# Kernel tuning notes

Hardware: AMD Instinct MI355X
Metric: run time of the kernel (lower is better)

Reference implementation:

```python
import jax, jax.numpy as jnp
import numpy as np

EPS = 1e-5

def mvn(feat):
    # instance norm with unbiased variance (torch .var default, correction=1)
    b, c, h, w = feat.shape
    x = feat.reshape(b, c, h * w)
    mean = x.mean(axis=2, keepdims=True)
    var = x.var(axis=2, ddof=1, keepdims=True) + EPS
    return ((x - mean) / jnp.sqrt(var)).reshape(b, c, h, w)

def conv1x1(x, w, bias):
    # x: [b,c,h,w], w: [o,c], bias: [o]
    return jnp.einsum('bchw,oc->bohw', x, w) + bias[None, :, None, None]

def setup_inputs() -> dict:
    key = jax.random.key(0)
    ks = jax.random.split(key, 10)
    C = 512
    content = jax.random.normal(ks[0], (4, C, 64, 64), dtype=jnp.float32)
    style = jax.random.normal(ks[1], (4, C, 64, 64), dtype=jnp.float32)
    s = 1.0 / np.sqrt(C)
    return {
        'content': content, 'style': style,
        'f_w': jax.random.normal(ks[2], (C, C), dtype=jnp.float32) * s,
        'f_b': jnp.zeros((C,), dtype=jnp.float32),
        'g_w': jax.random.normal(ks[3], (C, C), dtype=jnp.float32) * s,
        'g_b': jnp.zeros((C,), dtype=jnp.float32),
        'h_w': jax.random.normal(ks[4], (C, C), dtype=jnp.float32) * s,
        'h_b': jnp.zeros((C,), dtype=jnp.float32),
        'o_w': jax.random.normal(ks[5], (C, C), dtype=jnp.float32) * s,
        'o_b': jnp.zeros((C,), dtype=jnp.float32),
    }

def reference(content, style, f_w, f_b, g_w, g_b, h_w, h_b, o_w, o_b):
    b, c, hh, ww = content.shape
    F = conv1x1(mvn(content), f_w, f_b).reshape(b, c, hh * ww)   # [b,c,Nc]
    G = conv1x1(mvn(style), g_w, g_b).reshape(b, c, -1)          # [b,c,Ns]
    H = conv1x1(style, h_w, h_b).reshape(b, c, -1)               # [b,c,Ns]
    S = jnp.einsum('bcq,bcs->bqs', F, G)                          # [b,Nc,Ns]
    S = jax.nn.softmax(S, axis=-1)
    O = jnp.einsum('bcs,bqs->bcq', H, S).reshape(b, c, hh, ww)
    return conv1x1(O, o_w, o_b) + content
```

## Files before the change

### kernel.cpp

```cpp
#include <hip/hip_runtime.h>

constexpr int Cc = 512;
constexpr int Nn = 4096;
constexpr int Bb = 4;
#define EPS 1e-5f

using f16x8 = __attribute__((ext_vector_type(8))) _Float16;
using f32x4 = __attribute__((ext_vector_type(4))) float;
typedef unsigned short us;
typedef unsigned long long ull;

__device__ __forceinline__ us f2h(float f) {
    union { _Float16 h; us u; } v; v.h = (_Float16)f;
    return v.u;
}
__device__ __forceinline__ void gload_lds16(const void* g, void* l) {
    __builtin_amdgcn_global_load_lds(
        (const __attribute__((address_space(1))) void*)g,
        (__attribute__((address_space(3))) void*)l, 16, 0, 0);
}

__global__ __launch_bounds__(256) void stats2_kernel(const float* __restrict__ x0,
                                                     const float* __restrict__ x1,
                                                     float* __restrict__ mean0,
                                                     float* __restrict__ rstd0,
                                                     float* __restrict__ mean1,
                                                     float* __restrict__ rstd1) {
    int bc = blockIdx.x;
    const float* row;
    float *mean, *rstd;
    int idx;
    if (bc < Bb * Cc) { idx = bc; row = x0 + (size_t)idx * Nn; mean = mean0; rstd = rstd0; }
    else              { idx = bc - Bb * Cc; row = x1 + (size_t)idx * Nn; mean = mean1; rstd = rstd1; }
    float s = 0.f, sq = 0.f;
    for (int i = threadIdx.x * 4; i < Nn; i += 256 * 4) {
        float4 v = *reinterpret_cast<const float4*>(row + i);
        s  += v.x + v.y + v.z + v.w;
        sq += v.x*v.x + v.y*v.y + v.z*v.z + v.w*v.w;
    }
    for (int off = 32; off; off >>= 1) {
        s  += __shfl_down(s, off);
        sq += __shfl_down(sq, off);
    }
    __shared__ float ls[4], lsq[4];
    int wid = threadIdx.x >> 6;
    if ((threadIdx.x & 63) == 0) { ls[wid] = s; lsq[wid] = sq; }
    __syncthreads();
    if (threadIdx.x == 0) {
        float S  = ls[0] + ls[1] + ls[2] + ls[3];
        float SQ = lsq[0] + lsq[1] + lsq[2] + lsq[3];
        float m  = S / (float)Nn;
        float var = (SQ - S * m) / (float)(Nn - 1);
        mean[idx] = m;
        rstd[idx] = rsqrtf(var + EPS);
    }
}

__global__ __launch_bounds__(256) void pack_T(const float* __restrict__ X,
                                              const float* __restrict__ mean,
                                              const float* __restrict__ rstd,
                                              us* __restrict__ T0) {
    int b = blockIdx.z;
    int n0 = blockIdx.x * 64, c0 = blockIdx.y * 64;
    __shared__ float tile[64][65];
    const float* Xb = X + (size_t)b * Cc * Nn;
    for (int i = threadIdx.x; i < 64 * 64; i += 256) {
        int c = i >> 6, n = i & 63;
        float v = Xb[(size_t)(c0 + c) * Nn + n0 + n];
        int cg = b * Cc + c0 + c;
        tile[c][n] = (v - mean[cg]) * rstd[cg];
    }
    __syncthreads();
    us* Pb = T0 + (size_t)b * Nn * Cc;
    for (int i = threadIdx.x; i < 64 * 64; i += 256) {
        int n = i >> 6, c = i & 63;
        Pb[(size_t)(n0 + n) * Cc + c0 + c] = f2h(tile[c][n]);
    }
}

__global__ __launch_bounds__(256) void pack_style(const float* __restrict__ X,
                                                  const float* __restrict__ mean,
                                                  const float* __restrict__ rstd,
                                                  us* __restrict__ SNo,
                                                  us* __restrict__ SRo) {
    int b = blockIdx.z;
    int n0 = blockIdx.x * 64, c0 = blockIdx.y * 64;
    __shared__ float tile[64][65];
    const float* Xb = X + (size_t)b * Cc * Nn;
    for (int i = threadIdx.x; i < 64 * 64; i += 256) {
        int c = i >> 6, n = i & 63;
        tile[c][n] = Xb[(size_t)(c0 + c) * Nn + n0 + n];
    }
    __syncthreads();
    us* Nb = SNo + (size_t)b * Nn * Cc;
    us* Rb = SRo + (size_t)b * Nn * Cc;
    for (int i = threadIdx.x; i < 64 * 64; i += 256) {
        int n = i >> 6, c = i & 63;
        float raw = tile[c][n];
        int cg = b * Cc + c0 + c;
        size_t off = (size_t)(n0 + n) * Cc + c0 + c;
        Rb[off] = f2h(raw);
        Nb[off] = f2h((raw - mean[cg]) * rstd[cg]);
    }
}

__global__ __launch_bounds__(256) void pack_w(const float* __restrict__ fw, const float* __restrict__ gw,
                                              const float* __restrict__ hw, const float* __restrict__ ow,
                                              us* __restrict__ fo, us* __restrict__ go,
                                              us* __restrict__ ho, us* __restrict__ oo) {
    int i = blockIdx.x * 256 + threadIdx.x;
    if (i >= Cc * Cc) return;
    fo[i] = f2h(fw[i]);
    go[i] = f2h(gw[i]);
    ho[i] = f2h(hw[i]);
    oo[i] = f2h(ow[i]);
}

template <int EPI, int BIAS, bool RESID, int BM, int BN, int BK, int SWZ>
__global__ __launch_bounds__(256) void mfma_gemm(
    const us* __restrict__ A, int lda, long long strideA,
    const us* __restrict__ B, int ldb, long long strideB,
    void* __restrict__ out0, int ldc, long long strideC,
    const float* __restrict__ bias, const float* __restrict__ resid, long long strideR,
    int K) {
    constexpr int WM = BM / 2, WN = BN / 2;
    constexpr int MI = WM / 16, NI = WN / 16;
    constexpr int AE = BM * BK, BE = BN * BK;
    constexpr int BUFSZ = AE + BE;
    constexpr int ACH = AE / 512, BCH = BE / 512;
    __shared__ __attribute__((aligned(16))) us smem[2 * BUFSZ];

    int bz = blockIdx.z;
    const us* Ab = A + (size_t)bz * strideA;
    const us* Bbp = B + (size_t)bz * strideB;

    int bx = blockIdx.x, by = blockIdx.y;
    if constexpr (SWZ == 1) {
        int nwg = gridDim.x * gridDim.y;
        int bid = blockIdx.x + gridDim.x * blockIdx.y;
        int cpx = nwg >> 3;
        int swz = (bid & 7) * cpx + (bid >> 3);
        bx = swz % gridDim.x;
        by = swz / gridDim.x;
    } else if constexpr (SWZ == 2) {
        int bid = blockIdx.x + gridDim.x * blockIdx.y;
        int xcd = bid & 7;
        int idx = bid >> 3;
        int rpr = gridDim.y >> 2;
        int cpr = gridDim.x >> 1;
        int row0 = (xcd >> 1) * rpr;
        int col0 = (xcd & 1) * cpr;
        by = row0 + idx / cpr;
        bx = col0 + idx % cpr;
    }
    int m0 = by * BM, n0 = bx * BN;
    int tid = threadIdx.x, wave = tid >> 6, lane = tid & 63;
    int wr = wave >> 1, wc = wave & 1;
    int lr = lane & 15, lg = lane >> 4;

    auto stage = [&](int buf, int k0) {
        us* Asb = smem + buf * BUFSZ;
        us* Bsb = Asb + AE;
#pragma unroll
        for (int ch = wave; ch < ACH; ch += 4) {
            int e0 = ch * 512 + lane * 8;
            int kb = e0 / (BM * 32);
            int rem = e0 - kb * (BM * 32);
            int rr = rem >> 5;
            int gslot = ((rem & 31) >> 3) ^ ((rr >> 1) & 3);
            gload_lds16(Ab + (size_t)(m0 + rr) * lda + k0 + kb * 32 + gslot * 8,
                        Asb + ch * 512);
        }
#pragma unroll
        for (int ch = wave; ch < BCH; ch += 4) {
            int e0 = ch * 512 + lane * 8;
            int kb = e0 / (BN * 32);
            int rem = e0 - kb * (BN * 32);
            int rr = rem >> 5;
            int gslot = ((rem & 31) >> 3) ^ ((rr >> 1) & 3);
            gload_lds16(Bbp + (size_t)(n0 + rr) * ldb + k0 + kb * 32 + gslot * 8,
                        Bsb + ch * 512);
        }
    };

    f32x4 acc[MI][NI];
#pragma unroll
    for (int i = 0; i < MI; ++i)
#pragma unroll
        for (int j = 0; j < NI; ++j) acc[i][j] = (f32x4){0.f, 0.f, 0.f, 0.f};

    stage(0, 0);
    asm volatile("s_waitcnt vmcnt(0)" ::: "memory");
    __syncthreads();

    int nsteps = K / BK;
    for (int t = 0; t < nsteps; ++t) {
        int cur = t & 1;
        if (t + 1 < nsteps) stage(cur ^ 1, (t + 1) * BK);
        const us* As = smem + cur * BUFSZ;
        const us* Bs = As + AE;
#pragma unroll
        for (int kb = 0; kb < BK / 32; ++kb) {
            const us* Abase = As + kb * BM * 32;
            const us* Bbase = Bs + kb * BN * 32;
            f16x8 a[MI], b[NI];
#pragma unroll
            for (int x = 0; x < MI; ++x) {
                int row = wr * WM + x * 16 + lr;
                a[x] = *reinterpret_cast<const f16x8*>(
                    &Abase[row * 32 + ((lg ^ ((row >> 1) & 3)) << 3)]);
            }
#pragma unroll
            for (int x = 0; x < NI; ++x) {
                int row = wc * WN + x * 16 + lr;
                b[x] = *reinterpret_cast<const f16x8*>(
                    &Bbase[row * 32 + ((lg ^ ((row >> 1) & 3)) << 3)]);
            }
#pragma unroll
            for (int mi = 0; mi < MI; ++mi)
#pragma unroll
                for (int ni = 0; ni < NI; ++ni)
                    acc[mi][ni] = __builtin_amdgcn_mfma_f32_16x16x32_f16(a[mi], b[ni], acc[mi][ni], 0, 0, 0);
        }
        asm volatile("s_waitcnt vmcnt(0)" ::: "memory");
        __syncthreads();
    }

    constexpr int SP = BN + 4;
    float* sst = reinterpret_cast<float*>(smem);
    constexpr int CSEG = BN / 8;
    int rl = tid >> 3;
    int cb = (tid & 7) * CSEG;
#pragma unroll
    for (int mi = 0; mi < MI; ++mi) {
        __syncthreads();
#pragma unroll
        for (int ni = 0; ni < NI; ++ni) {
#pragma unroll
            for (int r = 0; r < 4; ++r)
                sst[(wr * 16 + lg * 4 + r) * SP + wc * WN + ni * 16 + lr] = acc[mi][ni][r];
        }
        __syncthreads();
        int grow = m0 + (rl >> 4) * WM + mi * 16 + (rl & 15);
        float bs = 0.f;
        if constexpr (BIAS == 1) bs = bias[grow];
#pragma unroll
        for (int j = 0; j < CSEG / 4; ++j) {
            int col = n0 + cb + j * 4;
            float4 v = *reinterpret_cast<const float4*>(&sst[rl * SP + cb + j * 4]);
            if constexpr (BIAS == 1) { v.x += bs; v.y += bs; v.z += bs; v.w += bs; }
            if constexpr (BIAS == 2) {
                const float4 bv = *reinterpret_cast<const float4*>(&bias[col]);
                v.x += bv.x; v.y += bv.y; v.z += bv.z; v.w += bv.w;
            }
            size_t off = (size_t)bz * strideC + (size_t)grow * ldc + col;
            if constexpr (RESID) {
                const float4 rr4 = *reinterpret_cast<const float4*>(
                    &resid[(size_t)bz * strideR + (size_t)grow * ldc + col]);
                v.x += rr4.x; v.y += rr4.y; v.z += rr4.z; v.w += rr4.w;
            }
            if constexpr (EPI == 0) {
                *reinterpret_cast<float4*>(&((float*)out0)[off]) = v;
            } else {
                ull pk = (ull)f2h(v.x) | ((ull)f2h(v.y) << 16)
                       | ((ull)f2h(v.z) << 32) | ((ull)f2h(v.w) << 48);
                *reinterpret_cast<ull*>(&((us*)out0)[off]) = pk;
            }
        }
    }
}

__global__ __launch_bounds__(256) void softmax_kernel(us* __restrict__ S) {
    us* rowp = S + (size_t)blockIdx.y * ((size_t)Nn * Nn) + (size_t)blockIdx.x * Nn;
    f16x8* r8 = reinterpret_cast<f16x8*>(rowp);
    int t = threadIdx.x;
    float f[16];
    float mx = -1e30f;
#pragma unroll
    for (int j = 0; j < 2; ++j) {
        f16x8 v = r8[t + 256 * j];
#pragma unroll
        for (int e = 0; e < 8; ++e) {
            f[j * 8 + e] = (float)v[e];
            mx = fmaxf(mx, f[j * 8 + e]);
        }
    }
    for (int off = 32; off; off >>= 1) mx = fmaxf(mx, __shfl_down(mx, off));
    __shared__ float redm[4], reds[4];
    int wid = t >> 6;
    if ((t & 63) == 0) redm[wid] = mx;
    __syncthreads();
    mx = fmaxf(fmaxf(redm[0], redm[1]), fmaxf(redm[2], redm[3]));
    float s = 0.f;
#pragma unroll
    for (int j = 0; j < 16; ++j) {
        f[j] = __expf(f[j] - mx);
        s += f[j];
    }
    for (int off = 32; off; off >>= 1) s += __shfl_down(s, off);
    if ((t & 63) == 0) reds[wid] = s;
    __syncthreads();
    s = reds[0] + reds[1] + reds[2] + reds[3];
    float inv = 1.f / s;
#pragma unroll
    for (int j = 0; j < 2; ++j) {
        f16x8 o;
#pragma unroll
        for (int e = 0; e < 8; ++e) o[e] = (_Float16)(f[j * 8 + e] * inv);
        r8[t + 256 * j] = o;
    }
}

extern "C" void kernel_launch(void* const* d_in, const int* in_sizes, int n_in,
                              void* d_out, int out_size, void* d_ws, size_t ws_size,
                              hipStream_t stream) {
    const float* content = (const float*)d_in[0];
    const float* style   = (const float*)d_in[1];
    const float* f_w = (const float*)d_in[2];
    const float* f_b = (const float*)d_in[3];
    const float* g_w = (const float*)d_in[4];
    const float* g_b = (const float*)d_in[5];
    const float* h_w = (const float*)d_in[6];
    const float* h_b = (const float*)d_in[7];
    const float* o_w = (const float*)d_in[8];
    const float* o_b = (const float*)d_in[9];
    float* out = (float*)d_out;
    char* ws = (char*)d_ws;

    const size_t PB   = (size_t)Cc * Nn;
    const size_t TEN  = PB * Bb;
    const size_t SMAT = (size_t)Nn * Nn;

    us* FT  = (us*)ws;
    us* GT  = FT + TEN;
    us* Hbf = GT + TEN;
    us* OT  = Hbf + TEN;
    us* fwh = OT + TEN;
    us* gwh = fwh + Cc * Cc;
    us* hwb = gwh + Cc * Cc;
    us* owb = hwb + Cc * Cc;
    float* meanC = (float*)(owb + Cc * Cc);
    float* rstdC = meanC + Bb * Cc;
    float* meanS = rstdC + Bb * Cc;
    float* rstdS = meanS + Bb * Cc;
    us* CN = (us*)(rstdS + Bb * Cc);
    us* SN = CN + TEN;
    us* SR = SN + TEN;
    us* S4 = CN;

    stats2_kernel<<<2 * Bb * Cc, 256, 0, stream>>>(content, style,
                                                   meanC, rstdC, meanS, rstdS);

    dim3 pgrid(Nn / 64, Cc / 64, Bb);
    pack_T<<<pgrid, 256, 0, stream>>>(content, meanC, rstdC, CN);
    pack_style<<<pgrid, 256, 0, stream>>>(style, meanS, rstdS, SN, SR);
    pack_w<<<(Cc * Cc + 255) / 256, 256, 0, stream>>>(f_w, g_w, h_w, o_w,
                                                      fwh, gwh, hwb, owb);

    mfma_gemm<1, 2, false, 64, 64, 64, 1><<<dim3(Cc / 64, Nn / 64, Bb), 256, 0, stream>>>(
        CN, Cc, (long long)PB, fwh, Cc, 0,
        FT, Cc, (long long)PB, f_b, nullptr, 0, Cc);
    mfma_gemm<1, 2, false, 64, 64, 64, 1><<<dim3(Cc / 64, Nn / 64, Bb), 256, 0, stream>>>(
        SN, Cc, (long long)PB, gwh, Cc, 0,
        GT, Cc, (long long)PB, g_b, nullptr, 0, Cc);
    mfma_gemm<1, 1, false, 64, 64, 64, 1><<<dim3(Nn / 64, Cc / 64, Bb), 256, 0, stream>>>(
        hwb, Cc, 0, SR, Cc, (long long)PB,
        Hbf, Nn, (long long)PB, h_b, nullptr, 0, Cc);

    mfma_gemm<1, 0, false, 128, 128, 32, 2><<<dim3(32, 32, Bb), 256, 0, stream>>>(
        FT, Cc, (long long)PB, GT, Cc, (long long)PB,
        S4, Nn, (long long)SMAT, nullptr, nullptr, 0, Cc);
    softmax_kernel<<<dim3(Nn, Bb), 256, 0, stream>>>(S4);
    mfma_gemm<1, 0, false, 128, 128, 64, 2><<<dim3(Cc / 128, Nn / 128, Bb), 256, 0, stream>>>(
        S4, Nn, (long long)SMAT, Hbf, Nn, (long long)PB,
        OT, Cc, (long long)PB, nullptr, nullptr, 0, Nn);

    mfma_gemm<0, 1, true, 64, 64, 64, 1><<<dim3(Nn / 64, Cc / 64, Bb), 256, 0, stream>>>(
        owb, Cc, 0, OT, Cc, (long long)PB,
        out, Nn, (long long)PB, o_b, content, (long long)PB, Cc);
}
```

Before: 332.4 us.

## Use 256x256-tile 8-wave MFMA GEMM with XCD-aware swizzle for score matrix

Adds a dedicated GEMM kernel for the F^T·G score computation that uses 256x256 block tiles with 512 threads (8 waves, 128x64 per wave), double-buffered LDS via direct global-to-LDS loads, and an XCD-aware block remapping. The larger tile raises arithmetic intensity per LDS load and the swizzle groups neighbouring tiles on the same XCD for L2 reuse. The epilogue writes scalar fp16 values with a strided pattern, which may coalesce poorly. The larger tile also uses more registers and LDS per block, which lowers occupancy.

New measurement: 326.4 us. Within noise of the previous version (-1.8%).

```diff
diff --git a/kernel.cpp b/kernel.cpp
--- a/kernel.cpp
+++ b/kernel.cpp
@@ -270,6 +270,115 @@
     }
 }
 
+template <int SWZ>
+__global__ __launch_bounds__(512) void mfma_gemm8w(
+    const us* __restrict__ A, int lda, long long strideA,
+    const us* __restrict__ B, int ldb, long long strideB,
+    us* __restrict__ out0, int ldc, long long strideC,
+    int K) {
+    constexpr int BM = 256, BN = 256, BK = 32;
+    constexpr int WM = 128, WN = 64;
+    constexpr int MI = WM / 16, NI = WN / 16;
+    constexpr int AE = BM * BK, BE = BN * BK;
+    constexpr int BUFSZ = AE + BE;
+    constexpr int ACH = AE / 512, BCH = BE / 512;
+    __shared__ __attribute__((aligned(16))) us smem[2 * BUFSZ];
+
+    int bz = blockIdx.z;
+    const us* Ab = A + (size_t)bz * strideA;
+    const us* Bbp = B + (size_t)bz * strideB;
+
+    int bx = blockIdx.x, by = blockIdx.y;
+    if constexpr (SWZ == 2) {
+        int bid = blockIdx.x + gridDim.x * blockIdx.y;
+        int xcd = bid & 7;
+        int idx = bid >> 3;
+        int rpr = gridDim.y >> 2;
+        int cpr = gridDim.x >> 1;
+        int row0 = (xcd >> 1) * rpr;
+        int col0 = (xcd & 1) * cpr;
+        by = row0 + idx / cpr;
+        bx = col0 + idx % cpr;
+    }
+    int m0 = by * BM, n0 = bx * BN;
+    int tid = threadIdx.x, wave = tid >> 6, lane = tid & 63;
+    int wr = wave >> 2, wc = wave & 3;
+    int lr = lane & 15, lg = lane >> 4;
+
+    auto stage = [&](int buf, int k0) {
+        us* Asb = smem + buf * BUFSZ;
+        us* Bsb = Asb + AE;
+#pragma unroll
+        for (int ch = wave; ch < ACH; ch += 8) {
+            int e0 = ch * 512 + lane * 8;
+            int rr = e0 >> 5;
+            int gslot = ((e0 & 31) >> 3) ^ ((rr >> 1) & 3);
+            gload_lds16(Ab + (size_t)(m0 + rr) * lda + k0 + gslot * 8,
+                        Asb + ch * 512);
+        }
+#pragma unroll
+        for (int ch = wave; ch < BCH; ch += 8) {
+            int e0 = ch * 512 + lane * 8;
+            int rr = e0 >> 5;
+            int gslot = ((e0 & 31) >> 3) ^ ((rr >> 1) & 3);
+            gload_lds16(Bbp + (size_t)(n0 + rr) * ldb + k0 + gslot * 8,
+                        Bsb + ch * 512);
+        }
+    };
+
+    f32x4 acc[MI][NI];
+#pragma unroll
+    for (int i = 0; i < MI; ++i)
+#pragma unroll
+        for (int j = 0; j < NI; ++j) acc[i][j] = (f32x4){0.f, 0.f, 0.f, 0.f};
+
+    stage(0, 0);
+    asm volatile("s_waitcnt vmcnt(0)" ::: "memory");
+    __syncthreads();
+
+    int nsteps = K / BK;
+    for (int t = 0; t < nsteps; ++t) {
+        int cur = t & 1;
+        if (t + 1 < nsteps) stage(cur ^ 1, (t + 1) * BK);
+        const us* As = smem + cur * BUFSZ;
+        const us* Bs = As + AE;
+        f16x8 a[MI], b[NI];
+#pragma unroll
+        for (int x = 0; x < MI; ++x) {
+            int row = wr * WM + x * 16 + lr;
+            a[x] = *reinterpret_cast<const f16x8*>(
+                &As[row * 32 + ((lg ^ ((row >> 1) & 3)) << 3)]);
+        }
+#pragma unroll
+        for (int x = 0; x < NI; ++x) {
+            int row = wc * WN + x * 16 + lr;
+            b[x] = *reinterpret_cast<const f16x8*>(
+                &Bs[row * 32 + ((lg ^ ((row >> 1) & 3)) << 3)]);
+        }
+#pragma unroll
+        for (int mi = 0; mi < MI; ++mi)
+#pragma unroll
+            for (int ni = 0; ni < NI; ++ni)
+                acc[mi][ni] = __builtin_amdgcn_mfma_f32_16x16x32_f16(a[mi], b[ni], acc[mi][ni], 0, 0, 0);
+        asm volatile("s_waitcnt vmcnt(0)" ::: "memory");
+        __syncthreads();
+    }
+
+#pragma unroll
+    for (int mi = 0; mi < MI; ++mi) {
+        int row = m0 + wr * WM + mi * 16 + lg * 4;
+#pragma unroll
+        for (int ni = 0; ni < NI; ++ni) {
+            int col = n0 + wc * WN + ni * 16 + lr;
+#pragma unroll
+            for (int r = 0; r < 4; ++r) {
+                size_t off = (size_t)bz * strideC + (size_t)(row + r) * ldc + col;
+                out0[off] = f2h(acc[mi][ni][r]);
+            }
+        }
+    }
+}
+
 __global__ __launch_bounds__(256) void softmax_kernel(us* __restrict__ S) {
     us* rowp = S + (size_t)blockIdx.y * ((size_t)Nn * Nn) + (size_t)blockIdx.x * Nn;
     f16x8* r8 = reinterpret_cast<f16x8*>(rowp);
@@ -367,9 +476,9 @@
         hwb, Cc, 0, SR, Cc, (long long)PB,
         Hbf, Nn, (long long)PB, h_b, nullptr, 0, Cc);
 
-    mfma_gemm<1, 0, false, 128, 128, 32, 2><<<dim3(32, 32, Bb), 256, 0, stream>>>(
+    mfma_gemm8w<2><<<dim3(Nn / 256, Nn / 256, Bb), 512, 0, stream>>>(
         FT, Cc, (long long)PB, GT, Cc, (long long)PB,
-        S4, Nn, (long long)SMAT, nullptr, nullptr, 0, Cc);
+        S4, Nn, (long long)SMAT, Cc);
     softmax_kernel<<<dim3(Nn, Bb), 256, 0, stream>>>(S4);
     mfma_gemm<1, 0, false, 128, 128, 64, 2><<<dim3(Cc / 128, Nn / 128, Bb), 256, 0, stream>>>(
         S4, Nn, (long long)SMAT, Hbf, Nn, (long long)PB,
```
